# Optimization experiments

Measured on AMD Instinct MI355X. Metric: run time of the kernel, lower is better.

Reference implementation:

```python
import jax, jax.numpy as jnp
import numpy as np

B, N = 64, 4096          # trees per batch, leaves per complete binary tree
V, S = 21, 50            # amino-acid vocab, grammar-symbol vocab
E, H = 64, 128           # embed_dim, hidden_dim


def setup_inputs() -> dict:
    key = jax.random.key(0)
    ks = jax.random.split(key, 16)

    def lin_w(k, din, dout):
        return (jax.random.normal(k, (dout, din), jnp.float32) / np.sqrt(din)).astype(jnp.float32)

    tokens = jax.random.randint(ks[0], (B, N), 0, V, dtype=jnp.int32)
    symbols = jax.random.randint(ks[1], (B, N - 1), 0, S, dtype=jnp.int32)

    emb = jax.random.normal(ks[2], (V, E), jnp.float32) * 0.02
    emb = emb.at[0].set(0.0)  # padding_idx=0
    sym_emb = jax.random.normal(ks[3], (S, E), jnp.float32) * 0.02

    return {
        "tokens": tokens, "symbols": symbols,
        "emb": emb, "sym_emb": sym_emb,
        "Wp": lin_w(ks[4], E, H), "bp": jnp.zeros((H,), jnp.float32),
        "Wi": lin_w(ks[5], H, H), "bi": jnp.zeros((H,), jnp.float32),
        "Ui": lin_w(ks[6], H, H),
        "Wf": lin_w(ks[7], H, H), "bf": jnp.zeros((H,), jnp.float32),
        "Uf": lin_w(ks[8], H, H),
        "Wo": lin_w(ks[9], H, H), "bo": jnp.zeros((H,), jnp.float32),
        "Uo": lin_w(ks[10], H, H),
        "Wu": lin_w(ks[11], H, H), "bu": jnp.zeros((H,), jnp.float32),
        "Uu": lin_w(ks[12], H, H),
        "Wout": lin_w(ks[13], H, H), "bout": jnp.zeros((H,), jnp.float32),
    }


def _encode(tokens, symbols, emb, sym_emb, Wp, bp, Wi, bi, Ui, Wf, bf, Uf,
            Wo, bo, Uo, Wu, bu, Uu, Wout, bout):
    emb = emb.at[0].set(0.0)  # padding row contributes nothing (and gets no grad)

    # Leaf nodes: amino-acid embedding -> input_proj, no children.
    x = emb[tokens] @ Wp.T + bp                      # [B, N, H]
    i = jax.nn.sigmoid(x @ Wi.T + bi)
    o = jax.nn.sigmoid(x @ Wo.T + bo)
    u = jnp.tanh(x @ Wu.T + bu)
    c = i * u                                        # [B, N, H]
    h = o * jnp.tanh(c)

    # Bottom-up over levels of the complete binary tree (Child-Sum Tree-LSTM).
    off, n = 0, N
    while n > 1:
        m = n // 2
        xs = sym_emb[symbols[:, off:off + m]] @ Wp.T + bp   # [B, m, H]
        hl, hr = h[:, 0::2], h[:, 1::2]
        cl, cr = c[:, 0::2], c[:, 1::2]
        ht = hl + hr                                         # h_tilde = sum_j h_j
        gi = jax.nn.sigmoid(xs @ Wi.T + bi + ht @ Ui.T)
        go = jax.nn.sigmoid(xs @ Wo.T + bo + ht @ Uo.T)
        gu = jnp.tanh(xs @ Wu.T + bu + ht @ Uu.T)
        fx = xs @ Wf.T + bf
        fl = jax.nn.sigmoid(fx + hl @ Uf.T)                  # per-child forget gates
        fr = jax.nn.sigmoid(fx + hr @ Uf.T)
        c = gi * gu + fl * cl + fr * cr
        h = go * jnp.tanh(c)
        off += m
        n = m

    root_h = h[:, 0]                                         # [B, H]
    return root_h @ Wout.T + bout                            # output_proj


def reference(tokens, symbols, emb, sym_emb, Wp, bp, Wi, bi, Ui, Wf, bf, Uf,
              Wo, bo, Uo, Wu, bu, Uu, Wout, bout):
    return _encode(tokens, symbols, emb, sym_emb, Wp, bp, Wi, bi, Ui, Wf, bf,
                   Uf, Wo, bo, Uo, Wu, bu, Uu, Wout, bout)
```

## Files before the change

kernel.cpp:

```cpp
#include <hip/hip_runtime.h>
#include <hip/hip_bf16.h>

typedef __attribute__((ext_vector_type(8))) short short8;
typedef __attribute__((ext_vector_type(4))) float f32x4;

static constexpr int B_ = 64;
static constexpr int N_ = 4096;
static constexpr int V_ = 21;
static constexpr int S_ = 50;
static constexpr int E_ = 64;
static constexpr int H_ = 128;
static constexpr int NPAIR = V_ * V_;
static constexpr int NTAB = NPAIR * S_;

__device__ __forceinline__ float rcp_(float x) { return __builtin_amdgcn_rcpf(x); }
__device__ __forceinline__ float sigm(float x) { return rcp_(1.0f + __expf(-x)); }
__device__ __forceinline__ float tanh_(float x) {
  float a = fabsf(x);
  float e = __expf(-2.0f * a);
  float t = (1.0f - e) * rcp_(1.0f + e);
  return x < 0.0f ? -t : t;
}
__device__ __forceinline__ unsigned short f2bf(float f) {
  __hip_bfloat16 b = __float2bfloat16(f);
  return *reinterpret_cast<unsigned short*>(&b);
}
__device__ __forceinline__ float bf2f(unsigned short u) {
  return __uint_as_float(((unsigned int)u) << 16);
}

struct Gates { float cv, hv; };
__device__ __forceinline__ Gates gate_combine(float4 sx,
    float i_p, float o_p, float u_p, float fl_p, float fr_p, float cl, float cr) {
  float gi = sigm(sx.x + i_p);
  float go = sigm(sx.y + o_p);
  float gu = tanh_(sx.z + u_p);
  float fl = sigm(sx.w + fl_p);
  float fr = sigm(sx.w + fr_p);
  float cv = fmaf(gi, gu, fmaf(fl, cl, fr * cr));
  Gates g; g.cv = cv; g.hv = go * tanh_(cv);
  return g;
}

__device__ __forceinline__ void bar_lds() {
  asm volatile("s_waitcnt lgkmcnt(0)" ::: "memory");
  __builtin_amdgcn_s_barrier();
  asm volatile("" ::: "memory");
}

__global__ void __launch_bounds__(512) k_pre(
    const float* __restrict__ Ui, const float* __restrict__ Uo,
    const float* __restrict__ Uu, const float* __restrict__ Uf,
    const float* __restrict__ Wi, const float* __restrict__ Wo,
    const float* __restrict__ Wu, const float* __restrict__ Wf,
    const float* __restrict__ Wp, const float* __restrict__ emb,
    const float* __restrict__ sym_emb,
    const float* __restrict__ bp, const float* __restrict__ bi,
    const float* __restrict__ bo, const float* __restrict__ bu,
    const float* __restrict__ bfv,
    const int* __restrict__ tokens, const int* __restrict__ symbols,
    unsigned short* __restrict__ Wfrag, float* __restrict__ leaf_c,
    float* __restrict__ symx, float* __restrict__ P_leaf,
    int* __restrict__ idx1) {
  __shared__ float x[128];
  __shared__ float zs[512];
  __shared__ float hl[128];
  int blk = blockIdx.x, t = threadIdx.x;
  if (blk < 16) {
    int idx = blk * 512 + t;
    int L = idx & 63;
    int K = (idx >> 6) & 3;
    int T = idx >> 8;
    int n = 16 * T + (L & 15);
    int k0 = 32 * K + ((L >> 4) << 3);
    int g = n >> 7, o = n & 127;
    const float* U = (g == 0) ? Ui : (g == 1) ? Uo : (g == 2) ? Uu : Uf;
    unsigned short out[8];
    #pragma unroll
    for (int j = 0; j < 8; ++j) out[j] = f2bf(U[o * 128 + k0 + j]);
    *(int4*)(Wfrag + (size_t)idx * 8) = *(int4*)out;
  } else if (blk < 16 + V_) {
    int v = blk - 16;
    if (t < 128) {
      float acc = bp[t];
      if (v != 0) {
        const float4* wr = (const float4*)(Wp + t * E_);
        const float4* er = (const float4*)(emb + v * E_);
        #pragma unroll 4
        for (int e4 = 0; e4 < E_ / 4; ++e4) {
          float4 w4 = wr[e4], e4v = er[e4];
          acc = fmaf(e4v.x, w4.x, acc); acc = fmaf(e4v.y, w4.y, acc);
          acc = fmaf(e4v.z, w4.z, acc); acc = fmaf(e4v.w, w4.w, acc);
        }
      }
      x[t] = acc;
    }
    __syncthreads();
    if (t < 384) {
      int g = t >> 7, o = t & 127;
      const float* bb = (g == 0) ? bi : (g == 1) ? bo : bu;
      const float* Wg = (g == 0) ? Wi : (g == 1) ? Wo : Wu;
      float z = bb[o];
      const float4* wr = (const float4*)(Wg + o * H_);
      #pragma unroll 4
      for (int k4 = 0; k4 < H_ / 4; ++k4) {
        float4 w4 = wr[k4];
        z = fmaf(x[4 * k4], w4.x, z); z = fmaf(x[4 * k4 + 1], w4.y, z);
        z = fmaf(x[4 * k4 + 2], w4.z, z); z = fmaf(x[4 * k4 + 3], w4.w, z);
      }
      zs[t] = z;
    }
    __syncthreads();
    if (t < 128) {
      float gi = sigm(zs[t]), go = sigm(zs[128 + t]), gu = tanh_(zs[256 + t]);
      float c = gi * gu;
      leaf_c[v * H_ + t] = c;
      unsigned short hb = f2bf(go * tanh_(c));
      hl[t] = bf2f(hb);
    }
    __syncthreads();
    {
      int g = t >> 7, o = t & 127;
      const float* Ug = (g == 0) ? Ui : (g == 1) ? Uo : (g == 2) ? Uu : Uf;
      float z = 0.f;
      const float4* wr = (const float4*)(Ug + o * H_);
      #pragma unroll 4
      for (int k4 = 0; k4 < H_ / 4; ++k4) {
        float4 w4 = wr[k4];
        z = fmaf(hl[4 * k4], w4.x, z); z = fmaf(hl[4 * k4 + 1], w4.y, z);
        z = fmaf(hl[4 * k4 + 2], w4.z, z); z = fmaf(hl[4 * k4 + 3], w4.w, z);
      }
      P_leaf[(size_t)v * 512 + t] = z;
    }
  } else if (blk < 16 + V_ + S_) {
    int s = blk - 16 - V_;
    if (t < 128) {
      float acc = bp[t];
      const float4* wr = (const float4*)(Wp + t * E_);
      const float4* er = (const float4*)(sym_emb + s * E_);
      #pragma unroll 4
      for (int e4 = 0; e4 < E_ / 4; ++e4) {
        float4 w4 = wr[e4], e4v = er[e4];
        acc = fmaf(e4v.x, w4.x, acc); acc = fmaf(e4v.y, w4.y, acc);
        acc = fmaf(e4v.z, w4.z, acc); acc = fmaf(e4v.w, w4.w, acc);
      }
      x[t] = acc;
    }
    __syncthreads();
    {
      int g = t >> 7, o = t & 127;
      const float* bb = (g == 0) ? bi : (g == 1) ? bo : (g == 2) ? bu : bfv;
      const float* Wg = (g == 0) ? Wi : (g == 1) ? Wo : (g == 2) ? Wu : Wf;
      float z = bb[o];
      const float4* wr = (const float4*)(Wg + o * H_);
      #pragma unroll 4
      for (int k4 = 0; k4 < H_ / 4; ++k4) {
        float4 w4 = wr[k4];
        z = fmaf(x[4 * k4], w4.x, z); z = fmaf(x[4 * k4 + 1], w4.y, z);
        z = fmaf(x[4 * k4 + 2], w4.z, z); z = fmaf(x[4 * k4 + 3], w4.w, z);
      }
      zs[t] = z;
    }
    __syncthreads();
    if (t < 128) {
      float4 v4 = make_float4(zs[t], zs[128 + t], zs[256 + t], zs[384 + t]);
      *(float4*)(symx + (size_t)s * 512 + t * 4) = v4;
    }
  } else {
    int g = (blk - 16 - V_ - S_) * 512 + t;
    int b = g >> 11, j = g & 2047;
    idx1[g] = (tokens[b * N_ + 2 * j] * V_ + tokens[b * N_ + 2 * j + 1]) * S_
              + symbols[b * (N_ - 1) + j];
  }
}

__global__ void k_tabB(const float* __restrict__ P_leaf, const float* __restrict__ symx,
                       const float* __restrict__ leaf_c,
                       unsigned short* __restrict__ tab_h8, float* __restrict__ tab_c) {
  int blk = blockIdx.x, t = threadIdx.x;
  int row = blk * 2 + (t >> 7);
  int u = t & 127;
  int p = row / S_, s = row - p * S_;
  int tl = p / V_, tr = p - tl * V_;
  const float* Pl = P_leaf + (size_t)tl * 512;
  const float* Pr = P_leaf + (size_t)tr * 512;
  float4 sx = *(const float4*)(symx + (size_t)s * 512 + u * 4);
  Gates gt = gate_combine(sx,
      Pl[u] + Pr[u], Pl[128 + u] + Pr[128 + u], Pl[256 + u] + Pr[256 + u],
      Pl[384 + u], Pr[384 + u],
      leaf_c[tl * H_ + u], leaf_c[tr * H_ + u]);
  tab_c[(size_t)row * H_ + u] = gt.cv;
  tab_h8[(size_t)row * H_ + u] = f2bf(gt.hv);
}

static constexpr int LVL23_CH = 16;
__global__ void __launch_bounds__(512) k_lvl23(
    const unsigned short* __restrict__ Wfrag, const float* __restrict__ symx,
    const int* __restrict__ symbols, const int* __restrict__ idx1,
    const unsigned short* __restrict__ gh8, const float* __restrict__ gc,
    unsigned short* __restrict__ h_out8, float* __restrict__ c_out) {
  __shared__ __align__(16) unsigned short Ag[2][32][136];
  __shared__ __align__(16) unsigned short Bh[16][136];
  __shared__ float Bc[16][132];
  const int t = threadIdx.x;
  const int w = t >> 6, L = t & 63, q = L >> 4, cL = L & 15;
  const int cc = 16 * w + cL;
  const int rowA = t >> 4, coA = (t & 15) * 8;

  const short8* wf = (const short8*)Wfrag;
  short8 bfr[4][4];
  #pragma unroll
  for (int K = 0; K < 4; ++K)
    #pragma unroll
    for (int g = 0; g < 4; ++g)
      bfr[g][K] = wf[(size_t)((w + 8 * g) * 4 + K) * 64 + L];

  const int t0 = blockIdx.x * LVL23_CH;

  int nn[4];
  #pragma unroll
  for (int it = 0; it < 4; ++it) nn[it] = 8 * (it >> 1) + 2 * q + (it & 1);

  int4 agv;
  float clp[4], crp[4];
  float4 sx1[4], sx2[2];
  {
    int gxr = idx1[t0 * 32 + rowA];
    agv = *(const int4*)(gh8 + (size_t)gxr * H_ + coA);
    const int* sb = symbols + (size_t)(t0 >> 6) * (N_ - 1);
    const int j20 = (t0 & 63) * 16;
    #pragma unroll
    for (int it = 0; it < 4; ++it) {
      int g2l = idx1[t0 * 32 + 2 * nn[it]];
      int g2r = idx1[t0 * 32 + 2 * nn[it] + 1];
      clp[it] = gc[(size_t)g2l * H_ + cc];
      crp[it] = gc[(size_t)g2r * H_ + cc];
      int sp = sb[2048 + j20 + nn[it]];
      sx1[it] = *(const float4*)(symx + (size_t)sp * 512 + cc * 4);
    }
    #pragma unroll
    for (int nd = 0; nd < 2; ++nd) {
      int sp = sb[3072 + (j20 >> 1) + 2 * q + nd];
      sx2[nd] = *(const float4*)(symx + (size_t)sp * 512 + cc * 4);
    }
  }

  for (int k = 0; k < LVL23_CH; ++k) {
    const int tile = t0 + k;
    const int buf = k & 1;
    const bool hasNext = (k + 1 < LVL23_CH);

    *(int4*)&Ag[buf][rowA][coA] = agv;
    bar_lds();

    int gxr_n = 0, g2l_n[4], g2r_n[4], sp1_n[4], sp2_n[2];
    if (hasNext) {
      const int tn = tile + 1;
      const int* sbn = symbols + (size_t)(tn >> 6) * (N_ - 1);
      const int j2n = (tn & 63) * 16;
      gxr_n = idx1[tn * 32 + rowA];
      #pragma unroll
      for (int it = 0; it < 4; ++it) {
        g2l_n[it] = idx1[tn * 32 + 2 * nn[it]];
        g2r_n[it] = idx1[tn * 32 + 2 * nn[it] + 1];
        sp1_n[it] = sbn[2048 + j2n + nn[it]];
      }
      sp2_n[0] = sbn[3072 + (j2n >> 1) + 2 * q];
      sp2_n[1] = sbn[3072 + (j2n >> 1) + 2 * q + 1];
    }

    f32x4 acc[2][4];
    #pragma unroll
    for (int r = 0; r < 2; ++r)
      #pragma unroll
      for (int g = 0; g < 4; ++g) acc[r][g] = (f32x4){0.f, 0.f, 0.f, 0.f};
    #pragma unroll
    for (int K = 0; K < 4; ++K) {
      short8 a0 = *(const short8*)&Ag[buf][cL][K * 32 + q * 8];
      short8 a1 = *(const short8*)&Ag[buf][16 + cL][K * 32 + q * 8];
      #pragma unroll
      for (int g = 0; g < 4; ++g) {
        acc[0][g] = __builtin_amdgcn_mfma_f32_16x16x32_bf16(a0, bfr[g][K], acc[0][g], 0, 0, 0);
        acc[1][g] = __builtin_amdgcn_mfma_f32_16x16x32_bf16(a1, bfr[g][K], acc[1][g], 0, 0, 0);
      }
    }
    float clp_n[4], crp_n[4];
    float4 sx1_n[4], sx2_n[2];
    if (hasNext) {
      agv = *(const int4*)(gh8 + (size_t)gxr_n * H_ + coA);
      #pragma unroll
      for (int it = 0; it < 4; ++it) {
        clp_n[it] = gc[(size_t)g2l_n[it] * H_ + cc];
        crp_n[it] = gc[(size_t)g2r_n[it] * H_ + cc];
        sx1_n[it] = *(const float4*)(symx + (size_t)sp1_n[it] * 512 + cc * 4);
      }
      sx2_n[0] = *(const float4*)(symx + (size_t)sp2_n[0] * 512 + cc * 4);
      sx2_n[1] = *(const float4*)(symx + (size_t)sp2_n[1] * 512 + cc * 4);
    }

    #pragma unroll
    for (int r = 0; r < 2; ++r) {
      #pragma unroll
      for (int nd = 0; nd < 2; ++nd) {
        int it = r * 2 + nd;
        int n = 8 * r + 2 * q + nd;
        Gates gt = gate_combine(sx1[it],
            acc[r][0][2 * nd] + acc[r][0][2 * nd + 1],
            acc[r][1][2 * nd] + acc[r][1][2 * nd + 1],
            acc[r][2][2 * nd] + acc[r][2][2 * nd + 1],
            acc[r][3][2 * nd], acc[r][3][2 * nd + 1], clp[it], crp[it]);
        Bc[n][cc] = gt.cv;
        Bh[n][cc] = f2bf(gt.hv);
      }
    }
    bar_lds();

    f32x4 acc2[4];
    #pragma unroll
    for (int g = 0; g < 4; ++g) acc2[g] = (f32x4){0.f, 0.f, 0.f, 0.f};
    #pragma unroll
    for (int K = 0; K < 4; ++K) {
      short8 a0 = *(const short8*)&Bh[cL][K * 32 + q * 8];
      #pragma unroll
      for (int g = 0; g < 4; ++g)
        acc2[g] = __builtin_amdgcn_mfma_f32_16x16x32_bf16(a0, bfr[g][K], acc2[g], 0, 0, 0);
    }
    #pragma unroll
    for (int nd = 0; nd < 2; ++nd) {
      int n = 2 * q + nd;
      int G3 = tile * 8 + n;
      Gates gt = gate_combine(sx2[nd],
          acc2[0][2 * nd] + acc2[0][2 * nd + 1],
          acc2[1][2 * nd] + acc2[1][2 * nd + 1],
          acc2[2][2 * nd] + acc2[2][2 * nd + 1],
          acc2[3][2 * nd], acc2[3][2 * nd + 1],
          Bc[2 * n][cc], Bc[2 * n + 1][cc]);
      c_out[(size_t)G3 * H_ + cc] = gt.cv;
      h_out8[(size_t)G3 * H_ + cc] = f2bf(gt.hv);
    }
    #pragma unroll
    for (int it = 0; it < 4; ++it) {
      clp[it] = clp_n[it]; crp[it] = crp_n[it]; sx1[it] = sx1_n[it];
    }
    sx2[0] = sx2_n[0]; sx2[1] = sx2_n[1];
  }
}

__global__ void __launch_bounds__(512) k_mid(
    const unsigned short* __restrict__ Wfrag, const float* __restrict__ symx,
    const int* __restrict__ symbols,
    const unsigned short* __restrict__ in_h8, const float* __restrict__ in_c,
    unsigned short* __restrict__ out_h8, float* __restrict__ out_c) {
  __shared__ __align__(16) unsigned short Ah0[64][136];
  __shared__ __align__(16) unsigned short Ah1[32][136];
  __shared__ float Cs0[64][128];
  __shared__ float Cs1[32][128];
  int t = threadIdx.x;
  int w = t >> 6, L = t & 63, q = L >> 4, cL = L & 15;
  int cc = 16 * w + cL;
  int blk = blockIdx.x;
  int b = blk >> 3, sub = blk & 7;
  size_t base3 = (size_t)blk * 64;

  const short8* wf = (const short8*)Wfrag;
  short8 bfr[4][4];
  #pragma unroll
  for (int K = 0; K < 4; ++K)
    #pragma unroll
    for (int g = 0; g < 4; ++g)
      bfr[g][K] = wf[(size_t)((w + 8 * g) * 4 + K) * 64 + L];

  #pragma unroll
  for (int i = 0; i < 2; ++i) {
    int fid = t + 512 * i;
    int row = fid >> 4, co = (fid & 15) * 8;
    *(int4*)&Ah0[row][co] = *(const int4*)(in_h8 + (base3 + row) * H_ + co);
  }
  #pragma unroll
  for (int i = 0; i < 4; ++i) {
    int fid = t + 512 * i;
    int row = fid >> 5, c4 = (fid & 31) << 2;
    *(float4*)&Cs0[row][c4] = *(const float4*)(in_c + (base3 + row) * H_ + c4);
  }
  __syncthreads();

  int R = 64;
  #pragma unroll
  for (int lev = 0; lev < 6; ++lev) {
    const int l = 4 + lev;
    const int nodes = R >> 1;
    const int jb = b * (N_ - 1) + (N_ - (N_ >> (l - 1))) + ((sub * 32) >> lev);
    unsigned short (*Ard)[136] = (lev & 1) ? Ah1 : Ah0;
    unsigned short (*Awr)[136] = (lev & 1) ? Ah0 : Ah1;
    const float* crd = (lev & 1) ? &Cs1[0][0] : &Cs0[0][0];
    float* cwr = (lev & 1) ? &Cs0[0][0] : &Cs1[0][0];
    const int nchunk = (nodes + 15) >> 4;
    for (int c = 0; c < nchunk; ++c) {
      int spre[4];
      #pragma unroll
      for (int it = 0; it < 4; ++it) {
        int n = 16 * c + 8 * (it >> 1) + 2 * q + (it & 1);
        spre[it] = (n < nodes) ? symbols[jb + n] : 0;
      }
      f32x4 acc[2][4];
      #pragma unroll
      for (int r = 0; r < 2; ++r)
        #pragma unroll
        for (int g = 0; g < 4; ++g) acc[r][g] = (f32x4){0.f, 0.f, 0.f, 0.f};
      const bool useA1 = (2 * nodes - 32 * c) > 16;
      #pragma unroll
      for (int K = 0; K < 4; ++K) {
        short8 a0 = *(const short8*)&Ard[32 * c + cL][K * 32 + q * 8];
        #pragma unroll
        for (int g = 0; g < 4; ++g)
          acc[0][g] = __builtin_amdgcn_mfma_f32_16x16x32_bf16(a0, bfr[g][K], acc[0][g], 0, 0, 0);
        if (useA1) {
          short8 a1 = *(const short8*)&Ard[32 * c + 16 + cL][K * 32 + q * 8];
          #pragma unroll
          for (int g = 0; g < 4; ++g)
            acc[1][g] = __builtin_amdgcn_mfma_f32_16x16x32_bf16(a1, bfr[g][K], acc[1][g], 0, 0, 0);
        }
      }
      #pragma unroll
      for (int r = 0; r < 2; ++r) {
        #pragma unroll
        for (int nd = 0; nd < 2; ++nd) {
          int it = r * 2 + nd;
          int n = 16 * c + 8 * r + 2 * q + nd;
          if (n < nodes) {
            float4 sx = *(const float4*)(symx + (size_t)spre[it] * 512 + cc * 4);
            Gates gt = gate_combine(sx,
                acc[r][0][2 * nd] + acc[r][0][2 * nd + 1],
                acc[r][1][2 * nd] + acc[r][1][2 * nd + 1],
                acc[r][2][2 * nd] + acc[r][2][2 * nd + 1],
                acc[r][3][2 * nd], acc[r][3][2 * nd + 1],
                crd[(size_t)(2 * n) * 128 + cc], crd[(size_t)(2 * n + 1) * 128 + cc]);
            if (lev == 5) {
              out_c[(size_t)blk * H_ + cc] = gt.cv;
              out_h8[(size_t)blk * H_ + cc] = f2bf(gt.hv);
            } else {
              cwr[(size_t)n * 128 + cc] = gt.cv;
              Awr[n][cc] = f2bf(gt.hv);
            }
          }
        }
      }
    }
    __syncthreads();
    R >>= 1;
  }
}

__global__ void __launch_bounds__(512, 2) k_fin(
    const unsigned short* __restrict__ Wfrag, const float* __restrict__ symx,
    const int* __restrict__ symbols,
    const unsigned short* __restrict__ in_h8, const float* __restrict__ in_c,
    const float* __restrict__ Wout, const float* __restrict__ bout,
    float* __restrict__ out) {
  __shared__ __align__(16) unsigned short Ah0[8][136];
  __shared__ __align__(16) unsigned short Ah1[4][136];
  __shared__ float Cs0[8][128];
  __shared__ float Cs1[4][128];
  __shared__ float rootv[128];
  int t = threadIdx.x;
  int w = t >> 6, L = t & 63, q = L >> 4, cL = L & 15;
  int cc = 16 * w + cL;
  int b = blockIdx.x;

  if (t < 128) {
    int row = t >> 4, co = (t & 15) * 8;
    *(int4*)&Ah0[row][co] = *(const int4*)(in_h8 + (size_t)(b * 8 + row) * H_ + co);
  }
  if (t < 256) {
    int row = t >> 5, c4 = (t & 31) << 2;
    *(float4*)&Cs0[row][c4] = *(const float4*)(in_c + (size_t)(b * 8 + row) * H_ + c4);
  }
  __syncthreads();

  const short8* wf = (const short8*)Wfrag;
  int R = 8;
  #pragma unroll
  for (int lev = 0; lev < 3; ++lev) {
    const int l = 10 + lev;
    const int nodes = R >> 1;
    const int jb = b * (N_ - 1) + (N_ - (N_ >> (l - 1)));
    unsigned short (*Ard)[136] = (lev & 1) ? Ah1 : Ah0;
    unsigned short (*Awr)[136] = (lev & 1) ? Ah0 : Ah1;
    const float* crd = (lev & 1) ? &Cs1[0][0] : &Cs0[0][0];
    float* cwr = (lev & 1) ? &Cs0[0][0] : &Cs1[0][0];
    int spre[4];
    #pragma unroll
    for (int it = 0; it < 4; ++it) {
      int n = 8 * (it >> 1) + 2 * q + (it & 1);
      spre[it] = (n < nodes) ? symbols[jb + n] : 0;
    }
    f32x4 acc[4];
    #pragma unroll
    for (int g = 0; g < 4; ++g) acc[g] = (f32x4){0.f, 0.f, 0.f, 0.f};
    #pragma unroll
    for (int K = 0; K < 4; ++K) {
      short8 bfr[4];
      #pragma unroll
      for (int g = 0; g < 4; ++g) bfr[g] = wf[(size_t)((w + 8 * g) * 4 + K) * 64 + L];
      short8 a0 = *(const short8*)&Ard[cL & 7][K * 32 + q * 8];
      #pragma unroll
      for (int g = 0; g < 4; ++g)
        acc[g] = __builtin_amdgcn_mfma_f32_16x16x32_bf16(a0, bfr[g], acc[g], 0, 0, 0);
    }
    #pragma unroll
    for (int nd = 0; nd < 2; ++nd) {
      int it = nd;
      int n = 2 * q + nd;
      if (n < nodes) {
        float4 sx = *(const float4*)(symx + (size_t)spre[it] * 512 + cc * 4);
        Gates gt = gate_combine(sx,
            acc[0][2 * nd] + acc[0][2 * nd + 1],
            acc[1][2 * nd] + acc[1][2 * nd + 1],
            acc[2][2 * nd] + acc[2][2 * nd + 1],
            acc[3][2 * nd], acc[3][2 * nd + 1],
            crd[(size_t)(2 * n) * 128 + cc], crd[(size_t)(2 * n + 1) * 128 + cc]);
        if (lev == 2) {
          rootv[cc] = gt.hv;
        } else {
          cwr[(size_t)n * 128 + cc] = gt.cv;
          Awr[n][cc] = f2bf(gt.hv);
        }
      }
    }
    __syncthreads();
    R >>= 1;
  }
  if (t < 128) {
    float acc = bout[t];
    const float4* wr = (const float4*)(Wout + t * H_);
    #pragma unroll 4
    for (int k4 = 0; k4 < H_ / 4; ++k4) {
      float4 w4 = wr[k4];
      acc = fmaf(rootv[4 * k4], w4.x, acc); acc = fmaf(rootv[4 * k4 + 1], w4.y, acc);
      acc = fmaf(rootv[4 * k4 + 2], w4.z, acc); acc = fmaf(rootv[4 * k4 + 3], w4.w, acc);
    }
    out[(size_t)b * H_ + t] = acc;
  }
}

extern "C" void kernel_launch(void* const* d_in, const int* in_sizes, int n_in,
                              void* d_out, int out_size, void* d_ws, size_t ws_size,
                              hipStream_t stream) {
  const int* tokens    = (const int*)d_in[0];
  const int* symbols   = (const int*)d_in[1];
  const float* emb     = (const float*)d_in[2];
  const float* sym_emb = (const float*)d_in[3];
  const float* Wp  = (const float*)d_in[4];
  const float* bp  = (const float*)d_in[5];
  const float* Wi  = (const float*)d_in[6];
  const float* bi  = (const float*)d_in[7];
  const float* Ui  = (const float*)d_in[8];
  const float* Wf  = (const float*)d_in[9];
  const float* bf  = (const float*)d_in[10];
  const float* Uf  = (const float*)d_in[11];
  const float* Wo  = (const float*)d_in[12];
  const float* bo  = (const float*)d_in[13];
  const float* Uo  = (const float*)d_in[14];
  const float* Wu  = (const float*)d_in[15];
  const float* bu  = (const float*)d_in[16];
  const float* Uu  = (const float*)d_in[17];
  const float* Wout= (const float*)d_in[18];
  const float* bout= (const float*)d_in[19];

  char* ws = (char*)d_ws;
  unsigned short* Wfrag   = (unsigned short*)(ws);
  float*          leaf_c  = (float*)(ws + 759040);
  float*          symx    = (float*)(ws + 769792);
  float*          P_leaf  = (float*)(ws + 872192);
  unsigned short* tab_h8  = (unsigned short*)(ws + 2001152UL);
  float*          tab_c   = (float*)(ws + 7645952UL);
  int*            idx1    = (int*)(ws + 18935552UL);
  unsigned short* L3h8    = (unsigned short*)(ws + 19459840UL);
  float*          L3c     = (float*)(ws + 27848448UL);
  unsigned short* L9h8    = (unsigned short*)(ws + 44625664UL);
  float*          L9c     = (float*)(ws + 44756736UL);

  k_pre<<<16 + V_ + S_ + 256, 512, 0, stream>>>(
      Ui, Uo, Uu, Uf, Wi, Wo, Wu, Wf, Wp, emb, sym_emb,
      bp, bi, bo, bu, bf, tokens, symbols,
      Wfrag, leaf_c, symx, P_leaf, idx1);
  k_tabB<<<NTAB / 2, 256, 0, stream>>>(P_leaf, symx, leaf_c, tab_h8, tab_c);
  k_lvl23<<<256, 512, 0, stream>>>(Wfrag, symx, symbols, idx1, tab_h8, tab_c,
                                   L3h8, L3c);
  k_mid<<<512, 512, 0, stream>>>(Wfrag, symx, symbols, L3h8, L3c, L9h8, L9c);
  k_fin<<<B_, 512, 0, stream>>>(Wfrag, symx, symbols, L9h8, L9c, Wout, bout,
                                (float*)d_out);
}
```

Measured before the change: 192.0 us.

## Double-buffer level-2/3 LDS staging and prefetch gathered h two tiles ahead

In the fused level-2/3 kernel, the staging buffers Bh and Bc are now double-buffered and the next tile's gathered h rows are written into the alternate Ag buffer before the mid-iteration barrier. This removes one of the two block barriers per tile. The gather of h for tile k+2 is issued right after the first MFMA pass, giving the load more time to land. The cost is extra LDS use and more live registers for the deeper prefetch, which could lower occupancy.

```diff
diff --git a/kernel.cpp b/kernel.cpp
--- a/kernel.cpp
+++ b/kernel.cpp
@@ -200,8 +200,8 @@
     const unsigned short* __restrict__ gh8, const float* __restrict__ gc,
     unsigned short* __restrict__ h_out8, float* __restrict__ c_out) {
   __shared__ __align__(16) unsigned short Ag[2][32][136];
-  __shared__ __align__(16) unsigned short Bh[16][136];
-  __shared__ float Bc[16][132];
+  __shared__ __align__(16) unsigned short Bh[2][16][136];
+  __shared__ float Bc[2][16][132];
   const int t = threadIdx.x;
   const int w = t >> 6, L = t & 63, q = L >> 4, cL = L & 15;
   const int cc = 16 * w + cL;
@@ -221,12 +221,15 @@
   #pragma unroll
   for (int it = 0; it < 4; ++it) nn[it] = 8 * (it >> 1) + 2 * q + (it & 1);
 
-  int4 agv;
+  int4 agv1;
   float clp[4], crp[4];
   float4 sx1[4], sx2[2];
   {
     int gxr = idx1[t0 * 32 + rowA];
-    agv = *(const int4*)(gh8 + (size_t)gxr * H_ + coA);
+    int4 agv0 = *(const int4*)(gh8 + (size_t)gxr * H_ + coA);
+    *(int4*)&Ag[0][rowA][coA] = agv0;
+    int gxr1 = idx1[(t0 + 1) * 32 + rowA];
+    agv1 = *(const int4*)(gh8 + (size_t)gxr1 * H_ + coA);
     const int* sb = symbols + (size_t)(t0 >> 6) * (N_ - 1);
     const int j20 = (t0 & 63) * 16;
     #pragma unroll
@@ -244,58 +247,54 @@
       sx2[nd] = *(const float4*)(symx + (size_t)sp * 512 + cc * 4);
     }
   }
+  bar_lds();
 
   for (int k = 0; k < LVL23_CH; ++k) {
     const int tile = t0 + k;
     const int buf = k & 1;
-    const bool hasNext = (k + 1 < LVL23_CH);
-
-    *(int4*)&Ag[buf][rowA][coA] = agv;
-    bar_lds();
-
-    int gxr_n = 0, g2l_n[4], g2r_n[4], sp1_n[4], sp2_n[2];
-    if (hasNext) {
+    const bool hasN1 = (k + 1 < LVL23_CH);
+    const bool hasN2 = (k + 2 < LVL23_CH);
+
+    f32x4 acc[2][4];
+    #pragma unroll
+    for (int r = 0; r < 2; ++r)
+      #pragma unroll
+      for (int g = 0; g < 4; ++g) acc[r][g] = (f32x4){0.f, 0.f, 0.f, 0.f};
+    #pragma unroll
+    for (int K = 0; K < 4; ++K) {
+      short8 a0 = *(const short8*)&Ag[buf][cL][K * 32 + q * 8];
+      short8 a1 = *(const short8*)&Ag[buf][16 + cL][K * 32 + q * 8];
+      #pragma unroll
+      for (int g = 0; g < 4; ++g) {
+        acc[0][g] = __builtin_amdgcn_mfma_f32_16x16x32_bf16(a0, bfr[g][K], acc[0][g], 0, 0, 0);
+        acc[1][g] = __builtin_amdgcn_mfma_f32_16x16x32_bf16(a1, bfr[g][K], acc[1][g], 0, 0, 0);
+      }
+    }
+
+    int4 agv2;
+    if (hasN2) {
+      int gxr2 = idx1[(tile + 2) * 32 + rowA];
+      agv2 = *(const int4*)(gh8 + (size_t)gxr2 * H_ + coA);
+    }
+    float clp_n[4], crp_n[4];
+    float4 sx1_n[4], sx2_n[2];
+    if (hasN1) {
       const int tn = tile + 1;
       const int* sbn = symbols + (size_t)(tn >> 6) * (N_ - 1);
       const int j2n = (tn & 63) * 16;
-      gxr_n = idx1[tn * 32 + rowA];
       #pragma unroll
       for (int it = 0; it < 4; ++it) {
-        g2l_n[it] = idx1[tn * 32 + 2 * nn[it]];
-        g2r_n[it] = idx1[tn * 32 + 2 * nn[it] + 1];
-        sp1_n[it] = sbn[2048 + j2n + nn[it]];
-      }
-      sp2_n[0] = sbn[3072 + (j2n >> 1) + 2 * q];
-      sp2_n[1] = sbn[3072 + (j2n >> 1) + 2 * q + 1];
-    }
-
-    f32x4 acc[2][4];
-    #pragma unroll
-    for (int r = 0; r < 2; ++r)
-      #pragma unroll
-      for (int g = 0; g < 4; ++g) acc[r][g] = (f32x4){0.f, 0.f, 0.f, 0.f};
-    #pragma unroll
-    for (int K = 0; K < 4; ++K) {
-      short8 a0 = *(const short8*)&Ag[buf][cL][K * 32 + q * 8];
-      short8 a1 = *(const short8*)&Ag[buf][16 + cL][K * 32 + q * 8];
-      #pragma unroll
-      for (int g = 0; g < 4; ++g) {
-        acc[0][g] = __builtin_amdgcn_mfma_f32_16x16x32_bf16(a0, bfr[g][K], acc[0][g], 0, 0, 0);
-        acc[1][g] = __builtin_amdgcn_mfma_f32_16x16x32_bf16(a1, bfr[g][K], acc[1][g], 0, 0, 0);
-      }
-    }
-    float clp_n[4], crp_n[4];
-    float4 sx1_n[4], sx2_n[2];
-    if (hasNext) {
-      agv = *(const int4*)(gh8 + (size_t)gxr_n * H_ + coA);
-      #pragma unroll
-      for (int it = 0; it < 4; ++it) {
-        clp_n[it] = gc[(size_t)g2l_n[it] * H_ + cc];
-        crp_n[it] = gc[(size_t)g2r_n[it] * H_ + cc];
-        sx1_n[it] = *(const float4*)(symx + (size_t)sp1_n[it] * 512 + cc * 4);
-      }
-      sx2_n[0] = *(const float4*)(symx + (size_t)sp2_n[0] * 512 + cc * 4);
-      sx2_n[1] = *(const float4*)(symx + (size_t)sp2_n[1] * 512 + cc * 4);
+        int g2l = idx1[tn * 32 + 2 * nn[it]];
+        int g2r = idx1[tn * 32 + 2 * nn[it] + 1];
+        clp_n[it] = gc[(size_t)g2l * H_ + cc];
+        crp_n[it] = gc[(size_t)g2r * H_ + cc];
+        int sp = sbn[2048 + j2n + nn[it]];
+        sx1_n[it] = *(const float4*)(symx + (size_t)sp * 512 + cc * 4);
+      }
+      int sp0 = sbn[3072 + (j2n >> 1) + 2 * q];
+      int sp1 = sbn[3072 + (j2n >> 1) + 2 * q + 1];
+      sx2_n[0] = *(const float4*)(symx + (size_t)sp0 * 512 + cc * 4);
+      sx2_n[1] = *(const float4*)(symx + (size_t)sp1 * 512 + cc * 4);
     }
 
     #pragma unroll
@@ -309,10 +308,12 @@
             acc[r][1][2 * nd] + acc[r][1][2 * nd + 1],
             acc[r][2][2 * nd] + acc[r][2][2 * nd + 1],
             acc[r][3][2 * nd], acc[r][3][2 * nd + 1], clp[it], crp[it]);
-        Bc[n][cc] = gt.cv;
-        Bh[n][cc] = f2bf(gt.hv);
-      }
-    }
+        Bc[buf][n][cc] = gt.cv;
+        Bh[buf][n][cc] = f2bf(gt.hv);
+      }
+    }
+    if (hasN1) *(int4*)&Ag[buf ^ 1][rowA][coA] = agv1;
+
     bar_lds();
 
     f32x4 acc2[4];
@@ -320,7 +321,7 @@
     for (int g = 0; g < 4; ++g) acc2[g] = (f32x4){0.f, 0.f, 0.f, 0.f};
     #pragma unroll
     for (int K = 0; K < 4; ++K) {
-      short8 a0 = *(const short8*)&Bh[cL][K * 32 + q * 8];
+      short8 a0 = *(const short8*)&Bh[buf][cL][K * 32 + q * 8];
       #pragma unroll
       for (int g = 0; g < 4; ++g)
         acc2[g] = __builtin_amdgcn_mfma_f32_16x16x32_bf16(a0, bfr[g][K], acc2[g], 0, 0, 0);
@@ -334,10 +335,11 @@
           acc2[1][2 * nd] + acc2[1][2 * nd + 1],
           acc2[2][2 * nd] + acc2[2][2 * nd + 1],
           acc2[3][2 * nd], acc2[3][2 * nd + 1],
-          Bc[2 * n][cc], Bc[2 * n + 1][cc]);
+          Bc[buf][2 * n][cc], Bc[buf][2 * n + 1][cc]);
       c_out[(size_t)G3 * H_ + cc] = gt.cv;
       h_out8[(size_t)G3 * H_ + cc] = f2bf(gt.hv);
     }
+    agv1 = agv2;
     #pragma unroll
     for (int it = 0; it < 4; ++it) {
       clp[it] = clp_n[it]; crp[it] = crp_n[it]; sx1[it] = sx1_n[it];
```

Result: no change. 192.9 us (+0.5%).
